# Kernel optimization log

Measured on AMD Instinct MI355X. Metric: run time of the kernel, lower is better.

Reference implementation:

```python
import jax, jax.numpy as jnp
import numpy as np

SEQ_LEN = 2048
D_MODEL = 1024
D_KEY = 64
BATCH = 8


def setup_inputs() -> dict:
    key = jax.random.key(0)
    ks = jax.random.split(key, 7)
    s = 1.0 / np.sqrt(D_MODEL)
    return {
        "input": jax.random.normal(ks[0], (BATCH, SEQ_LEN, D_MODEL), dtype=jnp.float32),
        "Wq": jax.random.uniform(ks[1], (D_MODEL, D_KEY), jnp.float32, -s, s),
        "bq": jax.random.uniform(ks[2], (D_KEY,), jnp.float32, -s, s),
        "Wk": jax.random.uniform(ks[3], (D_MODEL, D_KEY), jnp.float32, -s, s),
        "bk": jax.random.uniform(ks[4], (D_KEY,), jnp.float32, -s, s),
        "Wv": jax.random.uniform(ks[5], (D_MODEL, D_MODEL), jnp.float32, -s, s),
        "bv": jax.random.uniform(ks[6], (D_MODEL,), jnp.float32, -s, s),
    }


def reference(input, Wq, bq, Wk, bk, Wv, bv):
    # single-head causal attention with full score materialization
    q = input @ Wq + bq                      # [B, S, dk]
    k = input @ Wk + bk                      # [B, S, dk]
    v = input @ Wv + bv                      # [B, S, dm]
    scale = jnp.sqrt(jnp.asarray(D_KEY, input.dtype))
    scores = jnp.einsum("bqd,bkd->bqk", q, k) / scale   # [B, S, S]
    causal = jnp.tril(jnp.ones((SEQ_LEN, SEQ_LEN), dtype=bool))
    scores = jnp.where(causal[None, :, :], scores, -jnp.inf)
    attn = jax.nn.softmax(scores, axis=-1)
    return jnp.einsum("bqk,bkd->bqd", attn, v)           # [B, S, dm]
```

## Files before the change

### kernel.cpp

```cpp
#include <hip/hip_runtime.h>
#include <math.h>

#define B 8
#define S 2048
#define DM 1024
#define DK 64
#define M_ROWS (B*S)

typedef short s8v __attribute__((ext_vector_type(8)));
typedef float f4v __attribute__((ext_vector_type(4)));
typedef unsigned short us4 __attribute__((ext_vector_type(4)));

__device__ __forceinline__ unsigned short f2bf(float f) {
    union { float f; unsigned u; } v; v.f = f;
    unsigned r = v.u + 0x7fffu + ((v.u >> 16) & 1u);
    return (unsigned short)(r >> 16);
}
__device__ __forceinline__ s8v ld8(const unsigned short* p) {
    return *(const s8v*)p;
}
__device__ __forceinline__ f4v mf16(s8v a, s8v b, f4v c) {
    return __builtin_amdgcn_mfma_f32_16x16x32_bf16(a, b, c, 0, 0, 0);
}
__device__ __forceinline__ void gload16(const unsigned short* g, unsigned short* l) {
    __builtin_amdgcn_global_load_lds(
        (const __attribute__((address_space(1))) void*)g,
        (__attribute__((address_space(3))) void*)l, 16, 0, 0);
}

__global__ __launch_bounds__(256) void cast_x(const float* __restrict__ x,
                                              unsigned short* __restrict__ xb) {
    size_t i = ((size_t)blockIdx.x * 256 + threadIdx.x) * 4;
    float4 v = *(const float4*)(x + i);
    us4 o; o.x = f2bf(v.x); o.y = f2bf(v.y); o.z = f2bf(v.z); o.w = f2bf(v.w);
    *(us4*)(xb + i) = o;
}

__global__ __launch_bounds__(256) void wv_t(const float* __restrict__ Wv,
                                            unsigned short* __restrict__ Wvt) {
    __shared__ float T[32][33];
    int t = threadIdx.x;
    int k0 = blockIdx.y * 32, n0 = blockIdx.x * 32;
    int r = t >> 3, c = (t & 7) * 4;
    float4 v = *(const float4*)(Wv + (size_t)(k0 + r) * DM + n0 + c);
    T[r][c + 0] = v.x; T[r][c + 1] = v.y; T[r][c + 2] = v.z; T[r][c + 3] = v.w;
    __syncthreads();
    us4 o;
    o.x = f2bf(T[c + 0][r]); o.y = f2bf(T[c + 1][r]);
    o.z = f2bf(T[c + 2][r]); o.w = f2bf(T[c + 3][r]);
    *(us4*)(Wvt + (size_t)(n0 + r) * DM + k0 + c) = o;
}

__global__ __launch_bounds__(256) void wqk_t(const float* __restrict__ Wq,
                                             const float* __restrict__ Wk,
                                             unsigned short* __restrict__ Wqkt) {
    __shared__ float T[32][33];
    int t = threadIdx.x;
    int k0 = blockIdx.y * 32, n0 = blockIdx.x * 32;
    const float* src = (n0 < 64) ? Wq : Wk;
    int nc = (n0 < 64) ? n0 : (n0 - 64);
    int r = t >> 3, c = (t & 7) * 4;
    float4 v = *(const float4*)(src + (size_t)(k0 + r) * DK + nc + c);
    T[r][c + 0] = v.x; T[r][c + 1] = v.y; T[r][c + 2] = v.z; T[r][c + 3] = v.w;
    __syncthreads();
    us4 o;
    o.x = f2bf(T[c + 0][r]); o.y = f2bf(T[c + 1][r]);
    o.z = f2bf(T[c + 2][r]); o.w = f2bf(T[c + 3][r]);
    *(us4*)(Wqkt + (size_t)(n0 + r) * DM + k0 + c) = o;
}

__global__ __launch_bounds__(256) void qk_mfma(
        const unsigned short* __restrict__ xb,
        const unsigned short* __restrict__ Wqkt,
        const float* __restrict__ bq, const float* __restrict__ bk,
        unsigned short* __restrict__ Q, unsigned short* __restrict__ Ko) {
    __shared__ unsigned short XS[64 * 64];
    __shared__ unsigned short WS[128 * 64];
    int t = threadIdx.x;
    int w = t >> 6, lane = t & 63, l16 = lane & 15, quad = lane >> 4;
    int m0 = blockIdx.x * 64;
    int wm = (w >> 1) * 32, wn = (w & 1) * 64;
    f4v acc[2][4] = {};
    int srow = w * 8 + (lane >> 3);
    int scol = ((lane & 7) ^ (srow & 7)) * 8;
    int soff = w * 512 + lane * 8;
    for (int k0 = 0; k0 < DM; k0 += 64) {
        __syncthreads();
        #pragma unroll
        for (int i = 0; i < 2; ++i)
            gload16(xb + (size_t)(m0 + i * 32 + srow) * DM + k0 + scol,
                    XS + i * 2048 + soff);
        #pragma unroll
        for (int i = 0; i < 4; ++i)
            gload16(Wqkt + (size_t)(i * 32 + srow) * DM + k0 + scol,
                    WS + i * 2048 + soff);
        __syncthreads();
        #pragma unroll
        for (int ks = 0; ks < 2; ++ks) {
            s8v af[2], bf[4];
            #pragma unroll
            for (int i = 0; i < 2; ++i) {
                int r = wm + i * 16 + l16;
                af[i] = *(const s8v*)&XS[r * 64 + ((ks * 4 + quad) ^ (r & 7)) * 8];
            }
            #pragma unroll
            for (int j = 0; j < 4; ++j) {
                int r = wn + j * 16 + l16;
                bf[j] = *(const s8v*)&WS[r * 64 + ((ks * 4 + quad) ^ (r & 7)) * 8];
            }
            #pragma unroll
            for (int i = 0; i < 2; ++i)
                #pragma unroll
                for (int j = 0; j < 4; ++j)
                    acc[i][j] = mf16(af[i], bf[j], acc[i][j]);
        }
    }
    #pragma unroll
    for (int j = 0; j < 4; ++j) {
        int n = wn + j * 16 + l16;
        float bias = (n < 64) ? bq[n] : bk[n - 64];
        float scale = (n < 64) ? 0.125f : 1.0f;
        unsigned short* dst = (n < 64) ? Q : Ko;
        int nn = n & 63;
        #pragma unroll
        for (int i = 0; i < 2; ++i)
            #pragma unroll
            for (int rr = 0; rr < 4; ++rr) {
                int m = m0 + wm + i * 16 + quad * 4 + rr;
                dst[(size_t)m * DK + nn] = f2bf((acc[i][j][rr] + bias) * scale);
            }
    }
}

__global__ __launch_bounds__(256) void v_proj_mfma(
        const unsigned short* __restrict__ xb,
        const unsigned short* __restrict__ Wvt,
        const float* __restrict__ bv,
        unsigned short* __restrict__ Vt) {
    __shared__ unsigned short XS[128 * 64];
    __shared__ unsigned short WS[128 * 64];
    int t = threadIdx.x;
    int w = t >> 6, lane = t & 63, l16 = lane & 15, quad = lane >> 4;
    int m0 = blockIdx.y * 128, n0 = blockIdx.x * 128;
    int wm = (w >> 1) * 64, wn = (w & 1) * 64;
    f4v acc[4][4] = {};
    int srow = w * 8 + (lane >> 3);
    int scol = ((lane & 7) ^ (srow & 7)) * 8;
    int soff = w * 512 + lane * 8;
    for (int k0 = 0; k0 < DM; k0 += 64) {
        __syncthreads();
        #pragma unroll
        for (int i = 0; i < 4; ++i) {
            gload16(xb  + (size_t)(m0 + i * 32 + srow) * DM + k0 + scol,
                    XS + i * 2048 + soff);
            gload16(Wvt + (size_t)(n0 + i * 32 + srow) * DM + k0 + scol,
                    WS + i * 2048 + soff);
        }
        __syncthreads();
        #pragma unroll
        for (int ks = 0; ks < 2; ++ks) {
            s8v af[4], bf[4];
            #pragma unroll
            for (int i = 0; i < 4; ++i) {
                int r = wm + i * 16 + l16;
                af[i] = *(const s8v*)&XS[r * 64 + ((ks * 4 + quad) ^ (r & 7)) * 8];
            }
            #pragma unroll
            for (int j = 0; j < 4; ++j) {
                int r = wn + j * 16 + l16;
                bf[j] = *(const s8v*)&WS[r * 64 + ((ks * 4 + quad) ^ (r & 7)) * 8];
            }
            #pragma unroll
            for (int i = 0; i < 4; ++i)
                #pragma unroll
                for (int j = 0; j < 4; ++j)
                    acc[i][j] = mf16(af[i], bf[j], acc[i][j]);
        }
    }
    int bb = m0 >> 11;
    #pragma unroll
    for (int j = 0; j < 4; ++j) {
        int n = n0 + wn + j * 16 + l16;
        float bias = bv[n];
        #pragma unroll
        for (int i = 0; i < 4; ++i) {
            int m = m0 + wm + i * 16 + quad * 4;
            int s = m & (S - 1);
            us4 o;
            o.x = f2bf(acc[i][j][0] + bias); o.y = f2bf(acc[i][j][1] + bias);
            o.z = f2bf(acc[i][j][2] + bias); o.w = f2bf(acc[i][j][3] + bias);
            *(us4*)(Vt + ((size_t)bb * DM + n) * S + s) = o;
        }
    }
}

__global__ __launch_bounds__(512, 2) void attn_mfma(
        const unsigned short* __restrict__ Q,
        const unsigned short* __restrict__ K,
        const unsigned short* __restrict__ Vt,
        float* __restrict__ out) {
    __shared__ unsigned short PS[128][64];
    __shared__ float lS[128];
    __shared__ unsigned short VS[2][256][64];

    int t = threadIdx.x;
    int w = t >> 6, lane = t & 63;
    int l16 = lane & 15, hi = lane >> 4;
    int bid = blockIdx.x;
    int b  = bid & 7;
    int bx = (bid >> 3) & 3;
    int by = bid >> 5;
    int dm0 = bx * 256;
    int wn = (w & 3) * 64;
    int qg = (w >> 2) * 64;

    int vrow = t >> 3;
    int voff = t * 8;
    int gcol = ((t & 7) ^ ((t >> 3) & 7)) * 8;

    const unsigned short* Kb = K  + (size_t)b * S * DK;
    const unsigned short* Vb = Vt + ((size_t)b * DM + dm0) * S;
    const unsigned short* kbase = Kb + (size_t)l16 * DK + hi * 8;

    #pragma unroll 1
    for (int half = 0; half < 2; ++half) {
        int qidx = half ? (15 - by) : by;
        int q0 = qidx * 128;
        int NJ = q0 + 128;
        int qw = q0 + w * 16;

        s8v qf[2];
        #pragma unroll
        for (int ks = 0; ks < 2; ++ks)
            qf[ks] = ld8(Q + ((size_t)b * S + qw + l16) * DK + ks * 32 + hi * 8);

        float lacc = 0.f;
        f4v acc[4][4] = {};

        s8v ka[8];
        #pragma unroll
        for (int rep = 0; rep < 4; ++rep)
            gload16(Vb + (size_t)(rep * 64 + vrow) * S + gcol,
                    &VS[0][0][0] + rep * 4096 + voff);
        #pragma unroll
        for (int jt = 0; jt < 4; ++jt)
            #pragma unroll
            for (int ks = 0; ks < 2; ++ks)
                ka[jt * 2 + ks] = ld8(kbase + (size_t)(jt * 16) * DK + ks * 32);
        __syncthreads();

        int cur = 0;
        for (int j0 = 0; j0 < NJ; j0 += 64) {
            int jn = j0 + 64;
            bool pf = jn < NJ;
            if (pf) {
                #pragma unroll
                for (int rep = 0; rep < 4; ++rep)
                    gload16(Vb + (size_t)(rep * 64 + vrow) * S + jn + gcol,
                            &VS[cur ^ 1][0][0] + rep * 4096 + voff);
            }
            #pragma unroll
            for (int jt = 0; jt < 4; ++jt) {
                f4v d = {0.f, 0.f, 0.f, 0.f};
                d = mf16(ka[jt * 2 + 0], qf[0], d);
                d = mf16(ka[jt * 2 + 1], qf[1], d);
                int qglob = qw + l16;
                int jbase = j0 + jt * 16 + hi * 4;
                float p0 = (jbase + 0 <= qglob) ? __expf(d[0]) : 0.f;
                float p1 = (jbase + 1 <= qglob) ? __expf(d[1]) : 0.f;
                float p2 = (jbase + 2 <= qglob) ? __expf(d[2]) : 0.f;
                float p3 = (jbase + 3 <= qglob) ? __expf(d[3]) : 0.f;
                lacc += (p0 + p1) + (p2 + p3);
                unsigned r0, r1;
                asm("v_cvt_pk_bf16_f32 %0, %1, %2" : "=v"(r0) : "v"(p0), "v"(p1));
                asm("v_cvt_pk_bf16_f32 %0, %1, %2" : "=v"(r1) : "v"(p2), "v"(p3));
                int prow = w * 16 + l16;
                int pc = jt * 2 + (hi >> 1);
                uint2 pk2; pk2.x = r0; pk2.y = r1;
                *(uint2*)&PS[prow][((pc ^ (prow & 7)) * 8) + (hi & 1) * 4] = pk2;
            }
            if (pf) {
                #pragma unroll
                for (int jt = 0; jt < 4; ++jt)
                    #pragma unroll
                    for (int ks = 0; ks < 2; ++ks)
                        ka[jt * 2 + ks] =
                            ld8(kbase + (size_t)(jn + jt * 16) * DK + ks * 32);
            }
            __syncthreads();
            __builtin_amdgcn_s_setprio(1);
            #pragma unroll
            for (int js = 0; js < 2; ++js) {
                s8v pa[4];
                #pragma unroll
                for (int qt = 0; qt < 4; ++qt) {
                    int qr = qg + qt * 16 + l16;
                    pa[qt] = *(const s8v*)&PS[qr][((js * 4 + hi) ^ (qr & 7)) * 8];
                }
                #pragma unroll
                for (int nt = 0; nt < 4; ++nt) {
                    int nr = wn + nt * 16 + l16;
                    s8v vb = *(const s8v*)&VS[cur][nr][((js * 4 + hi) ^ (nr & 7)) * 8];
                    #pragma unroll
                    for (int qt = 0; qt < 4; ++qt)
                        acc[qt][nt] = mf16(pa[qt], vb, acc[qt][nt]);
                }
            }
            __builtin_amdgcn_s_setprio(0);
            __syncthreads();
            cur ^= 1;
        }

        {
            float lt = lacc;
            lt += __shfl_xor(lt, 16);
            lt += __shfl_xor(lt, 32);
            if (hi == 0) lS[w * 16 + l16] = lt;
        }
        __syncthreads();

        #pragma unroll
        for (int qt = 0; qt < 4; ++qt) {
            f4v lv = *(const f4v*)&lS[qg + qt * 16 + hi * 4];
            f4v inv;
            inv[0] = 1.f / lv[0]; inv[1] = 1.f / lv[1];
            inv[2] = 1.f / lv[2]; inv[3] = 1.f / lv[3];
            size_t rbase = (size_t)b * S + q0 + qg + qt * 16 + hi * 4;
            #pragma unroll
            for (int nt = 0; nt < 4; ++nt)
                #pragma unroll
                for (int r = 0; r < 4; ++r)
                    out[(rbase + r) * DM + dm0 + wn + nt * 16 + l16] =
                        acc[qt][nt][r] * inv[r];
        }
        __syncthreads();
    }
}

extern "C" void kernel_launch(void* const* d_in, const int* in_sizes, int n_in,
                              void* d_out, int out_size, void* d_ws, size_t ws_size,
                              hipStream_t stream) {
    const float* x  = (const float*)d_in[0];
    const float* Wq = (const float*)d_in[1];
    const float* bq = (const float*)d_in[2];
    const float* Wk = (const float*)d_in[3];
    const float* bk = (const float*)d_in[4];
    const float* Wv = (const float*)d_in[5];
    const float* bv = (const float*)d_in[6];
    float* out = (float*)d_out;

    unsigned short* xb   = (unsigned short*)d_ws;
    unsigned short* Wvt  = xb   + (size_t)M_ROWS * DM;
    unsigned short* Qb   = Wvt  + (size_t)DM * DM;
    unsigned short* Kb   = Qb   + (size_t)M_ROWS * DK;
    unsigned short* Vt   = Kb   + (size_t)M_ROWS * DK;
    unsigned short* Wqkt = Vt   + (size_t)B * DM * S;

    cast_x<<<(size_t)M_ROWS * DM / 1024, 256, 0, stream>>>(x, xb);
    wv_t<<<dim3(32, 32), 256, 0, stream>>>(Wv, Wvt);
    wqk_t<<<dim3(4, 32), 256, 0, stream>>>(Wq, Wk, Wqkt);
    qk_mfma<<<M_ROWS / 64, 256, 0, stream>>>(xb, Wqkt, bq, bk, Qb, Kb);
    v_proj_mfma<<<dim3(DM / 128, M_ROWS / 128), 256, 0, stream>>>(xb, Wvt, bv, Vt);
    attn_mfma<<<dim3(256), 512, 0, stream>>>(Qb, Kb, Vt, out);
}
```

Baseline: 280.4 us.

## Double-buffer P tile to drop a barrier and coalesce Vt epilogue stores

The attention loop now double-buffers the P tile in shared memory. This lets each iteration use a single __syncthreads instead of two, and the prefetch of the next V tile and K fragments moves to after that barrier. Separately, the V-projection MFMA operands are swapped so that lanes index consecutive sequence positions in the epilogue. Writes to the transposed Vt then coalesce along S, at the cost of 2-byte scalar stores and one vector bias load. The trade-offs are extra LDS for the second P buffer and a tighter dependence on the async V loads having completed at the single barrier.

```diff
diff --git a/kernel.cpp b/kernel.cpp
--- a/kernel.cpp
+++ b/kernel.cpp
@@ -174,22 +174,21 @@
             for (int i = 0; i < 4; ++i)
                 #pragma unroll
                 for (int j = 0; j < 4; ++j)
-                    acc[i][j] = mf16(af[i], bf[j], acc[i][j]);
+                    acc[i][j] = mf16(bf[j], af[i], acc[i][j]);
         }
     }
     int bb = m0 >> 11;
     #pragma unroll
     for (int j = 0; j < 4; ++j) {
-        int n = n0 + wn + j * 16 + l16;
-        float bias = bv[n];
+        int nb = n0 + wn + j * 16 + quad * 4;
+        f4v bias4 = *(const f4v*)&bv[nb];
         #pragma unroll
         for (int i = 0; i < 4; ++i) {
-            int m = m0 + wm + i * 16 + quad * 4;
-            int s = m & (S - 1);
-            us4 o;
-            o.x = f2bf(acc[i][j][0] + bias); o.y = f2bf(acc[i][j][1] + bias);
-            o.z = f2bf(acc[i][j][2] + bias); o.w = f2bf(acc[i][j][3] + bias);
-            *(us4*)(Vt + ((size_t)bb * DM + n) * S + s) = o;
+            int s = (m0 + wm + i * 16 + l16) & (S - 1);
+            #pragma unroll
+            for (int r = 0; r < 4; ++r)
+                Vt[((size_t)bb * DM + nb + r) * S + s] =
+                    f2bf(acc[i][j][r] + bias4[r]);
         }
     }
 }
@@ -199,7 +198,7 @@
         const unsigned short* __restrict__ K,
         const unsigned short* __restrict__ Vt,
         float* __restrict__ out) {
-    __shared__ unsigned short PS[128][64];
+    __shared__ unsigned short PS[2][128][64];
     __shared__ float lS[128];
     __shared__ unsigned short VS[2][256][64];
 
@@ -247,18 +246,9 @@
             #pragma unroll
             for (int ks = 0; ks < 2; ++ks)
                 ka[jt * 2 + ks] = ld8(kbase + (size_t)(jt * 16) * DK + ks * 32);
-        __syncthreads();
-
-        int cur = 0;
+
         for (int j0 = 0; j0 < NJ; j0 += 64) {
-            int jn = j0 + 64;
-            bool pf = jn < NJ;
-            if (pf) {
-                #pragma unroll
-                for (int rep = 0; rep < 4; ++rep)
-                    gload16(Vb + (size_t)(rep * 64 + vrow) * S + jn + gcol,
-                            &VS[cur ^ 1][0][0] + rep * 4096 + voff);
-            }
+            int jj = (j0 >> 6) & 1;
             #pragma unroll
             for (int jt = 0; jt < 4; ++jt) {
                 f4v d = {0.f, 0.f, 0.f, 0.f};
@@ -277,9 +267,15 @@
                 int prow = w * 16 + l16;
                 int pc = jt * 2 + (hi >> 1);
                 uint2 pk2; pk2.x = r0; pk2.y = r1;
-                *(uint2*)&PS[prow][((pc ^ (prow & 7)) * 8) + (hi & 1) * 4] = pk2;
-            }
-            if (pf) {
+                *(uint2*)&PS[jj][prow][((pc ^ (prow & 7)) * 8) + (hi & 1) * 4] = pk2;
+            }
+            __syncthreads();
+            int jn = j0 + 64;
+            if (jn < NJ) {
+                #pragma unroll
+                for (int rep = 0; rep < 4; ++rep)
+                    gload16(Vb + (size_t)(rep * 64 + vrow) * S + jn + gcol,
+                            &VS[jj ^ 1][0][0] + rep * 4096 + voff);
                 #pragma unroll
                 for (int jt = 0; jt < 4; ++jt)
                     #pragma unroll
@@ -287,7 +283,6 @@
                         ka[jt * 2 + ks] =
                             ld8(kbase + (size_t)(jn + jt * 16) * DK + ks * 32);
             }
-            __syncthreads();
             __builtin_amdgcn_s_setprio(1);
             #pragma unroll
             for (int js = 0; js < 2; ++js) {
@@ -295,20 +290,18 @@
                 #pragma unroll
                 for (int qt = 0; qt < 4; ++qt) {
                     int qr = qg + qt * 16 + l16;
-                    pa[qt] = *(const s8v*)&PS[qr][((js * 4 + hi) ^ (qr & 7)) * 8];
+                    pa[qt] = *(const s8v*)&PS[jj][qr][((js * 4 + hi) ^ (qr & 7)) * 8];
                 }
                 #pragma unroll
                 for (int nt = 0; nt < 4; ++nt) {
                     int nr = wn + nt * 16 + l16;
-                    s8v vb = *(const s8v*)&VS[cur][nr][((js * 4 + hi) ^ (nr & 7)) * 8];
+                    s8v vb = *(const s8v*)&VS[jj][nr][((js * 4 + hi) ^ (nr & 7)) * 8];
                     #pragma unroll
                     for (int qt = 0; qt < 4; ++qt)
                         acc[qt][nt] = mf16(pa[qt], vb, acc[qt][nt]);
                 }
             }
             __builtin_amdgcn_s_setprio(0);
-            __syncthreads();
-            cur ^= 1;
         }
 
         {
```

Result: slower. 295.0 us (+5.2%).
